# Performance work log

Hardware: AMD Instinct MI355X
Metric: run time of the kernel (lower is better)

The kernel has to match this reference:

```python
import jax, jax.numpy as jnp
import numpy as np

DIM = 1024
NH = 8
HD = DIM // NH  # 128
E = 8
EPS = 1e-5


def rope_cos_sin(L, hd):
    # matches RotaryPositionEmbedding: emb = cat([freqs, freqs], -1)
    inv_freq = 1.0 / (10000.0 ** (jnp.arange(0, hd, 2, dtype=jnp.float32) / hd))
    freqs = jnp.arange(L, dtype=jnp.float32)[:, None] * inv_freq[None, :]  # (L, hd/2)
    emb = jnp.concatenate([freqs, freqs], axis=-1)  # (L, hd)
    return jnp.cos(emb), jnp.sin(emb)


def rotate_half(x):
    # interleaved rotate, as in the torch apply_rope
    x1 = x[..., 0::2]
    x2 = x[..., 1::2]
    return jnp.stack((-x2, x1), axis=-1).reshape(x.shape)


def rope(t, cos, sin):
    # t: (B,H,L,D); cos/sin: (L,D)
    return t * cos[None, None] + rotate_half(t) * sin[None, None]


def heads(t):
    B, L, C = t.shape
    return t.reshape(B, L, NH, HD).transpose(0, 2, 1, 3)  # (B,H,L,D)


def setup_inputs() -> dict:
    key = jax.random.key(0)
    ks = jax.random.split(key, 32)
    std = 0.02
    d = {}
    d['x'] = jax.random.normal(ks[0], (16, 512, DIM), jnp.float32)
    d['h_a'] = jax.random.normal(ks[1], (16, 256, DIM), jnp.float32)
    d['h_t'] = jax.random.normal(ks[2], (16, 256, DIM), jnp.float32)
    names = ['qa', 'ka', 'va', 'qt', 'kt', 'vt', 'o', 'ffn']
    for i, n in enumerate(names):
        d['W_' + n] = jax.random.normal(ks[3 + 2 * i], (E, DIM, DIM), jnp.float32) * std
        d['b_' + n] = jax.random.normal(ks[4 + 2 * i], (E, DIM), jnp.float32) * std
    d['gamma'] = jnp.ones((E, DIM), jnp.float32)
    d['beta'] = jnp.zeros((E, DIM), jnp.float32)
    d['gating_factor'] = jnp.zeros((E,), jnp.float32)
    d['expert_idx'] = 3
    return d


def reference(x, h_a, h_t,
              W_qa, b_qa, W_ka, b_ka, W_va, b_va,
              W_qt, b_qt, W_kt, b_kt, W_vt, b_vt,
              W_o, b_o, W_ffn, b_ffn,
              gamma, beta, gating_factor, expert_idx):
    e = expert_idx

    def lin(t, W, b):
        return t @ W[e].T + b[e]

    B, T, C = x.shape
    Ka = h_a.shape[1]
    Kt = h_t.shape[1]

    q_a = heads(lin(x, W_qa, b_qa))        # (B,H,T,D)
    q_t = heads(lin(x, W_qt, b_qt))
    k_a = heads(lin(h_a, W_ka, b_ka))      # (B,H,Ka,D)
    v_a = heads(lin(h_a, W_va, b_va))
    k_t = heads(lin(h_t, W_kt, b_kt))      # (B,H,Kt,D)
    v_t = heads(lin(h_t, W_vt, b_vt))

    cos_m, sin_m = rope_cos_sin(T, HD)
    q_a = rope(q_a, cos_m, sin_m)
    q_t = rope(q_t, cos_m, sin_m)
    cos_a, sin_a = rope_cos_sin(Ka, HD)
    k_a = rope(k_a, cos_a, sin_a)
    cos_t, sin_t = rope_cos_sin(Kt, HD)
    k_t = rope(k_t, cos_t, sin_t)

    ratio_g = jax.nn.sigmoid(gating_factor[e])
    s_a = jnp.einsum('bhtd,bhkd->bhtk', q_a, k_a)
    s_t = jnp.einsum('bhtd,bhkd->bhtk', q_t, k_t) * ratio_g
    scores = jnp.concatenate([s_a, s_t], axis=-1) / np.sqrt(HD)
    w = jax.nn.softmax(scores, axis=-1)            # (B,H,T,Ka+Kt)
    v = jnp.concatenate([v_a, v_t], axis=2)        # (B,H,Ka+Kt,D)
    out = jnp.einsum('bhtk,bhkd->bhtd', w, v)
    out = out.transpose(0, 2, 1, 3).reshape(B, T, C)
    out = lin(out, W_o, b_o)

    x = out + x
    # ffn: SmileMoENorm -> SmileMoELinear -> ReLU (no extra residual)
    mu = jnp.mean(x, axis=-1, keepdims=True)
    var = jnp.var(x, axis=-1, keepdims=True)
    xn = (x - mu) / jnp.sqrt(var + EPS) * gamma[e] + beta[e]
    x = jax.nn.relu(lin(xn, W_ffn, b_ffn))
    return x
```

## Files before the change

### kernel.cpp

```cpp
#include <hip/hip_runtime.h>
#include <stdint.h>

typedef __bf16 bf16x8 __attribute__((ext_vector_type(8)));
typedef float f32x4 __attribute__((ext_vector_type(4)));
typedef unsigned short u16x8 __attribute__((ext_vector_type(8)));

typedef const __attribute__((address_space(1))) void* gas_ptr;
typedef __attribute__((address_space(3))) void* las_ptr;
typedef const __attribute__((address_space(3))) char* lds_c3;

__device__ __forceinline__ void gload16(const void* g, void* l) {
  __builtin_amdgcn_global_load_lds((gas_ptr)g, (las_ptr)l, 16, 0, 0);
}

__device__ __forceinline__ bf16x8 dsread16(const char* p) {
  bf16x8 r;
  asm volatile("ds_read_b128 %0, %1" : "=v"(r) : "v"((lds_c3)p));
  return r;
}
__device__ __forceinline__ void dswrite2(char* p, uint32_t v) {
  asm volatile("ds_write_b16 %0, %1" : : "v"((las_ptr)p), "v"(v));
}
template <int OFF>
__device__ __forceinline__ float dswz(float x) {
  float r;
  asm volatile("ds_swizzle_b32 %0, %1 offset:%c2" : "=v"(r) : "v"(x), "i"(OFF));
  return r;
}

__device__ __forceinline__ unsigned short f2bf(float f) {
  uint32_t u = __float_as_uint(f);
  u += 0x7FFFu + ((u >> 16) & 1u);
  return (unsigned short)(u >> 16);
}

#define SB __builtin_amdgcn_sched_barrier(0)
#define BAR __builtin_amdgcn_s_barrier()
#define LGK0 asm volatile("s_waitcnt lgkmcnt(0)")

__device__ __forceinline__ void conv8(const float* __restrict__ src,
                                      unsigned short* __restrict__ dst, int i) {
  const float4* s4 = (const float4*)src;
  float4 a = s4[2 * i], b = s4[2 * i + 1];
  u16x8 r;
  r[0] = f2bf(a.x); r[1] = f2bf(a.y); r[2] = f2bf(a.z); r[3] = f2bf(a.w);
  r[4] = f2bf(b.x); r[5] = f2bf(b.y); r[6] = f2bf(b.z); r[7] = f2bf(b.w);
  *(u16x8*)&dst[(size_t)i * 8] = r;
}

__global__ __launch_bounds__(256)
void prep_all(const float* __restrict__ x, const float* __restrict__ h_a,
              const float* __restrict__ h_t,
              const float* W0, const float* W1, const float* W2, const float* W3,
              const float* W4, const float* W5, const float* W6, const float* W7,
              const int* __restrict__ eptr,
              unsigned short* __restrict__ XB, unsigned short* __restrict__ HAB,
              unsigned short* __restrict__ HTB, unsigned short* __restrict__ WW,
              float* __restrict__ cosb, float* __restrict__ sinb) {
  const int blk = blockIdx.x, tid = threadIdx.x;
  if (blk < 4096) {
    conv8(x, XB, blk * 256 + tid);
  } else if (blk < 6144) {
    conv8(h_a, HAB, (blk - 4096) * 256 + tid);
  } else if (blk < 8192) {
    conv8(h_t, HTB, (blk - 6144) * 256 + tid);
  } else if (blk < 12288) {
    const int w = (blk - 8192) >> 9;
    const int i = ((blk - 8192) & 511) * 256 + tid;
    const float* wp;
    switch (w) {
      case 0: wp = W0; break; case 1: wp = W1; break;
      case 2: wp = W2; break; case 3: wp = W3; break;
      case 4: wp = W4; break; case 5: wp = W5; break;
      case 6: wp = W6; break; default: wp = W7; break;
    }
    conv8(wp + (size_t)(*eptr) * 1048576, WW + (size_t)w * 1048576, i);
  } else {
    const int i = (blk - 12288) * 256 + tid;
    const int t = i >> 7, d = i & 127;
    const int f = d & 63;
    float invf = expf(-0.14391156831212787f * (float)f);
    float ang = (float)t * invf;
    float s, c;
    sincosf(ang, &s, &c);
    cosb[i] = c;
    sinb[i] = s;
  }
}

template <int MODE>
__global__ __launch_bounds__(512, 1)
void gemm3r(const unsigned short* __restrict__ A0, const unsigned short* __restrict__ A1,
            const unsigned short* __restrict__ W0, const unsigned short* __restrict__ W1,
            const unsigned short* __restrict__ W2, const unsigned short* __restrict__ W3,
            const float* __restrict__ bias0, const float* __restrict__ bias1,
            const float* __restrict__ bias2, const float* __restrict__ bias3,
            const int* __restrict__ eptr, const float* __restrict__ ctab,
            const float* __restrict__ stab,
            unsigned short* __restrict__ out0, unsigned short* __restrict__ out1,
            unsigned short* __restrict__ outV,
            const float* __restrict__ resid, float* __restrict__ outf) {
  __shared__ __align__(16) char AL[98304];
  __shared__ __align__(16) char BL[49152];
  const int tid = threadIdx.x;
  const int lane = tid & 63, wid = tid >> 6, fr = lane & 15, g = lane >> 4;
  const int wm = wid >> 1, wn = wid & 1;
  const int id = blockIdx.x;
  constexpr int CPX = (MODE == 0) ? 64 : 32;
  const int swz = (id & 7) * CPX + (id >> 3);
  constexpr int NBNS = (MODE <= 1) ? 4 : 3;
  const int bm = swz >> NBNS;
  const int bn = swz & ((1 << NBNS) - 1);
  const int z = (MODE == 1) ? blockIdx.y : 0;
  const int e = *eptr;

  const unsigned short* Asel;
  const unsigned short* Wsel;
  const float* bias;
  int half = 0, cb0;
  if constexpr (MODE == 0) {
    Asel = A0;
    half = bn >> 3;
    Wsel = half ? W1 : W0;
    bias = (half ? bias1 : bias0) + e * 1024;
    cb0 = (bn & 7) * 128;
  } else if constexpr (MODE == 1) {
    Asel = z ? A1 : A0;
    half = bn >> 3;
    Wsel = z ? (half ? W3 : W2) : (half ? W1 : W0);
    bias = (z ? (half ? bias3 : bias2) : (half ? bias1 : bias0)) + e * 1024;
    cb0 = (bn & 7) * 128;
  } else {
    Asel = A0;
    Wsel = W0;
    bias = bias0 + e * 1024;
    cb0 = bn * 128;
  }

  const char* Ab = (const char*)Asel + (size_t)bm * 256 * 2048;
  const char* Bb = (const char*)Wsel + (size_t)cb0 * 2048;

  const int csw = (((tid & 7) ^ ((tid >> 3) & 7)) << 4);
  const char* Ags = Ab + (tid >> 3) * 2048 + csw;
  const char* Bgs = Bb + (tid >> 3) * 2048 + csw;
  char* Ald = AL + tid * 16;
  char* Bld = BL + tid * 16;

#define STA(T, BUF)                                                         \
  { const char* s_ = Ags + (T) * 128;                                       \
    char* d_ = Ald + (BUF) * 32768;                                         \
    gload16(s_, d_);                  gload16(s_ + 131072, d_ + 8192);      \
    gload16(s_ + 262144, d_ + 16384); gload16(s_ + 393216, d_ + 24576); }
#define STB(T, BUF)                                                         \
  { const char* s_ = Bgs + (T) * 128;                                       \
    char* d_ = Bld + (BUF) * 16384;                                         \
    gload16(s_, d_);                  gload16(s_ + 131072, d_ + 8192); }

  const int lsw7 = fr & 7;
  const int ksel = (wid & 4) ? 4 : 0;
  const int cA = ((ksel + g) ^ lsw7) << 4;
  const int cB = (((4 - ksel) + g) ^ lsw7) << 4;
  const int arow = (wm * 64 + fr) * 128;
  const int brow = (wn * 64 + fr) * 128;

  f32x4 acc[4][4];
#pragma unroll
  for (int m = 0; m < 4; ++m)
#pragma unroll
    for (int n = 0; n < 4; ++n) acc[m][n] = f32x4{0.f, 0.f, 0.f, 0.f};
  bf16x8 af[4], bf[4];

#define RDAB(BASEA, BASEB, C)                                               \
  { const char* pa_ = (BASEA) + arow + (C);                                 \
    const char* pb_ = (BASEB) + brow + (C);                                 \
    _Pragma("unroll") for (int m = 0; m < 4; ++m)                           \
        af[m] = dsread16(pa_ + m * 2048);                                   \
    _Pragma("unroll") for (int n = 0; n < 4; ++n)                           \
        bf[n] = dsread16(pb_ + n * 2048); }

#define MF16                                                                \
  __builtin_amdgcn_s_setprio(1);                                            \
  _Pragma("unroll") for (int m = 0; m < 4; ++m)                             \
    _Pragma("unroll") for (int n = 0; n < 4; ++n)                           \
        acc[m][n] = __builtin_amdgcn_mfma_f32_16x16x32_bf16(                \
            af[m], bf[n], acc[m][n], 0, 0, 0);                              \
  __builtin_amdgcn_s_setprio(0);

  STA(0, 0); STB(0, 0); STA(1, 1); STB(1, 1);

  int bc = 0;
#pragma unroll 1
  for (int t = 0; t < 16; ++t) {
    SB;
    if (t <= 14) asm volatile("s_waitcnt vmcnt(6)");
    else         asm volatile("s_waitcnt vmcnt(0)");
    BAR; SB;
    const char* ALc = AL + bc * 32768;
    const char* BLc = BL + bc * 16384;
    const int bs = bc ? bc - 1 : 2;
    RDAB(ALc, BLc, cA); SB;
    if (t <= 13) STA(t + 2, bs);
    SB; LGK0; SB;
    MF16 SB;
    RDAB(ALc, BLc, cB); SB;
    if (t <= 13) STB(t + 2, bs);
    SB; LGK0; SB;
    MF16 SB;
    bc = (bc == 2) ? 0 : bc + 1;
  }
#undef RDAB
#undef MF16
#undef STA
#undef STB

  const int wrow0 = bm * 256 + wm * 64;
#pragma unroll
  for (int m = 0; m < 4; ++m) {
#pragma unroll
    for (int n = 0; n < 4; ++n) {
      const int lc = wn * 64 + n * 16 + fr;
      const int gc = cb0 + lc;
      const float bv = bias[gc];
#pragma unroll
      for (int j = 0; j < 4; ++j) {
        const int grow = wrow0 + m * 16 + g * 4 + j;
        float v = acc[m][n][j] + bv;
        if constexpr (MODE == 0) {
          const int t = grow & 511, bb = grow >> 9;
          const int hh = gc >> 7, dd = gc & 127;
          float pv = __shfl_xor(v, 1);
          float cs = ctab[t * 128 + dd], sn = stab[t * 128 + dd];
          float rh = (dd & 1) ? pv : -pv;
          float o = v * cs + rh * sn;
          unsigned short* dst = half ? out1 : out0;
          dst[(((size_t)(bb * 8 + hh) * 512 + t) << 7) + dd] = f2bf(o);
        } else if constexpr (MODE == 1) {
          const int t = grow & 255, bb = grow >> 8;
          const int hh = gc >> 7, dd = gc & 127;
          if (half == 0) {
            float pv = __shfl_xor(v, 1);
            float cs = ctab[t * 128 + dd], sn = stab[t * 128 + dd];
            float rh = (dd & 1) ? pv : -pv;
            float o = v * cs + rh * sn;
            unsigned short* dst = z ? out1 : out0;
            dst[(((size_t)(bb * 8 + hh) * 256 + t) << 7) + dd] = f2bf(o);
          } else {
            outV[(((size_t)(bb * 8 + hh) << 7) + dd) * 512 + z * 256 + t] = f2bf(v);
          }
        } else {
          const size_t idx = ((size_t)grow << 10) + gc;
          if constexpr (MODE == 2) outf[idx] = v + resid[idx];
          else outf[idx] = fmaxf(v, 0.f);
        }
      }
    }
  }
}

__global__ __launch_bounds__(256, 2)
void attn_kernel(const unsigned short* __restrict__ QA, const unsigned short* __restrict__ QT,
                 const unsigned short* __restrict__ KA, const unsigned short* __restrict__ KT,
                 const unsigned short* __restrict__ VT,
                 unsigned short* __restrict__ AO,
                 const float* __restrict__ gating, const int* __restrict__ eptr) {
  __shared__ unsigned short Ks[2][8192];
  __shared__ unsigned short Vs[2][8192];
  __shared__ unsigned short Ps[8192];
  const int tid = threadIdx.x, lane = tid & 63, wv = tid >> 6;
  const int fr = lane & 15, g = lane >> 4;
  const int bid = blockIdx.x;
  const int b = bid >> 5, h = (bid >> 2) & 7, q0 = (bid & 3) << 7;
  const float ratio = 1.f / (1.f + __expf(-gating[*eptr]));
  const float SC = 0.08838834764831845f;
  const size_t bh = (size_t)(b * 8 + h);

  bf16x8 qf[2][4];
  {
    const char* qa = (const char*)QA + ((bh * 512 + q0 + wv * 32 + fr) << 8) + g * 16;
#pragma unroll
    for (int mb = 0; mb < 2; ++mb)
#pragma unroll
      for (int kb = 0; kb < 4; ++kb)
        qf[mb][kb] = *(const bf16x8*)(qa + mb * 4096 + kb * 64);
  }

  auto stage = [&](int t, int buf) {
    const char* kgb = (const char*)((t < 4) ? KA : KT) + ((bh * 256 + ((size_t)(t & 3) << 6)) << 8);
    const char* vgb = (const char*)VT + (bh << 17) + (t << 7);
    char* ksd = (char*)Ks[buf] + tid * 16;
    char* vsd = (char*)Vs[buf] + tid * 16;
#pragma unroll
    for (int j = 0; j < 4; ++j) {
      const int rk = j * 16 + (tid >> 4);
      const int ck = ((tid & 15) << 4) ^ ((rk & 7) << 4);
      gload16(kgb + rk * 256 + ck, ksd + j * 4096);
      const int dv = j * 32 + (tid >> 3);
      const int cv = ((tid & 7) << 4) ^ ((dv & 7) << 4);
      gload16(vgb + dv * 1024 + cv, vsd + j * 4096);
    }
  };

  float m_run[2][4], l_run[2][4];
  f32x4 oacc[2][8];
#pragma unroll
  for (int mb = 0; mb < 2; ++mb) {
#pragma unroll
    for (int j = 0; j < 4; ++j) { m_run[mb][j] = -1e30f; l_run[mb][j] = 0.f; }
#pragma unroll
    for (int db = 0; db < 8; ++db) oacc[mb][db] = f32x4{0.f, 0.f, 0.f, 0.f};
  }

  stage(0, 0);

  for (int it = 0; it < 8; ++it) {
    const int cur = it & 1;
    if (it < 7) stage(it + 1, cur ^ 1);
    SB;
    if (it < 7) asm volatile("s_waitcnt vmcnt(8)");
    else        asm volatile("s_waitcnt vmcnt(0)");
    SB;
    BAR;
    SB;

    if (it == 4) {
      const char* qt = (const char*)QT + ((bh * 512 + q0 + wv * 32 + fr) << 8) + g * 16;
#pragma unroll
      for (int mb = 0; mb < 2; ++mb)
#pragma unroll
        for (int kb = 0; kb < 4; ++kb)
          qf[mb][kb] = *(const bf16x8*)(qt + mb * 4096 + kb * 64);
    }
    const float sc = (it < 4) ? SC : SC * ratio;
    const char* kc = (const char*)Ks[cur];
    const char* vc = (const char*)Vs[cur];

    f32x4 s[2][4];
#pragma unroll
    for (int mb = 0; mb < 2; ++mb)
#pragma unroll
      for (int nb = 0; nb < 4; ++nb) s[mb][nb] = f32x4{0.f, 0.f, 0.f, 0.f};
    bf16x8 kfa[4], kfb[4];
#pragma unroll
    for (int kb = 0; kb < 4; ++kb) {
      const int byt = (fr * 256 + kb * 64 + g * 16) ^ ((fr & 7) << 4);
      kfa[kb] = dsread16(kc + byt);
    }
#pragma unroll
    for (int nb = 0; nb < 4; ++nb) {
      if (nb < 3) {
#pragma unroll
        for (int kb = 0; kb < 4; ++kb) {
          const int r = (nb + 1) * 16 + fr;
          const int byt = (r * 256 + kb * 64 + g * 16) ^ ((r & 7) << 4);
          if (nb & 1) kfa[kb] = dsread16(kc + byt);
          else        kfb[kb] = dsread16(kc + byt);
        }
        asm volatile("s_waitcnt lgkmcnt(4)");
      } else {
        asm volatile("s_waitcnt lgkmcnt(0)");
      }
      SB;
      __builtin_amdgcn_s_setprio(1);
#pragma unroll
      for (int kb = 0; kb < 4; ++kb) {
        bf16x8 kf = (nb & 1) ? kfb[kb] : kfa[kb];
        s[0][nb] = __builtin_amdgcn_mfma_f32_16x16x32_bf16(qf[0][kb], kf, s[0][nb], 0, 0, 0);
        s[1][nb] = __builtin_amdgcn_mfma_f32_16x16x32_bf16(qf[1][kb], kf, s[1][nb], 0, 0, 0);
      }
      __builtin_amdgcn_s_setprio(0);
    }
    SB;

    float red[8];
#pragma unroll
    for (int mb = 0; mb < 2; ++mb)
#pragma unroll
      for (int j = 0; j < 4; ++j) {
        float mx = -1e30f;
#pragma unroll
        for (int nb = 0; nb < 4; ++nb) {
          s[mb][nb][j] *= sc;
          mx = fmaxf(mx, s[mb][nb][j]);
        }
        red[mb * 4 + j] = mx;
      }
#define MAXR(OFF)                                                        \
    { float tmp[8];                                                      \
      _Pragma("unroll") for (int k = 0; k < 8; ++k) tmp[k] = dswz<OFF>(red[k]); \
      asm volatile("s_waitcnt lgkmcnt(0)");                              \
      SB;                                                                \
      _Pragma("unroll") for (int k = 0; k < 8; ++k) red[k] = fmaxf(red[k], tmp[k]); }
    MAXR(0x041F) MAXR(0x081F) MAXR(0x101F) MAXR(0x201F)
#undef MAXR
#pragma unroll
    for (int mb = 0; mb < 2; ++mb)
#pragma unroll
      for (int j = 0; j < 4; ++j) {
        const float mn = fmaxf(m_run[mb][j], red[mb * 4 + j]);
        const float alpha = __expf(m_run[mb][j] - mn);
        m_run[mb][j] = mn;
        l_run[mb][j] *= alpha;
#pragma unroll
        for (int db = 0; db < 8; ++db) oacc[mb][db][j] *= alpha;
      }
#pragma unroll
    for (int mb = 0; mb < 2; ++mb)
#pragma unroll
      for (int nb = 0; nb < 4; ++nb)
#pragma unroll
        for (int j = 0; j < 4; ++j) {
          float p = __expf(s[mb][nb][j] - m_run[mb][j]);
          l_run[mb][j] += p;
          const int r = wv * 32 + mb * 16 + g * 4 + j;
          const int byt = (r * 128 + (nb * 16 + fr) * 2) ^ ((r & 7) << 4);
          dswrite2((char*)Ps + byt, (uint32_t)f2bf(p));
        }

#pragma unroll
    for (int kb2 = 0; kb2 < 2; ++kb2) {
      bf16x8 pf[2], vf[8];
#pragma unroll
      for (int mb = 0; mb < 2; ++mb) {
        const int r = wv * 32 + mb * 16 + fr;
        const int byt = (r * 128 + kb2 * 64 + g * 16) ^ ((r & 7) << 4);
        pf[mb] = dsread16((const char*)Ps + byt);
      }
#pragma unroll
      for (int db = 0; db < 8; ++db) {
        const int rv = db * 16 + fr;
        const int byt = (rv * 128 + kb2 * 64 + g * 16) ^ ((rv & 7) << 4);
        vf[db] = dsread16(vc + byt);
      }
      asm volatile("s_waitcnt lgkmcnt(0)");
      SB;
      __builtin_amdgcn_s_setprio(1);
#pragma unroll
      for (int db = 0; db < 8; ++db) {
        oacc[0][db] = __builtin_amdgcn_mfma_f32_16x16x32_bf16(pf[0], vf[db], oacc[0][db], 0, 0, 0);
        oacc[1][db] = __builtin_amdgcn_mfma_f32_16x16x32_bf16(pf[1], vf[db], oacc[1][db], 0, 0, 0);
      }
      __builtin_amdgcn_s_setprio(0);
    }
    SB;
    BAR;
  }

#pragma unroll
  for (int mb = 0; mb < 2; ++mb)
#pragma unroll
    for (int j = 0; j < 4; ++j) {
      float lt = l_run[mb][j];
#pragma unroll
      for (int d = 1; d < 16; d <<= 1) lt += __shfl_xor(lt, d);
      float inv = 1.f / lt;
#pragma unroll
      for (int db = 0; db < 8; ++db) {
        float o = oacc[mb][db][j] * inv;
        int row = q0 + wv * 32 + mb * 16 + g * 4 + j;
        int col = h * 128 + db * 16 + fr;
        AO[(((size_t)b * 512 + row) << 10) + col] = f2bf(o);
      }
    }
}

__global__ __launch_bounds__(256)
void ln_kernel(const float* __restrict__ X2, const float* __restrict__ gbase,
               const float* __restrict__ bbase, const int* __restrict__ eptr,
               unsigned short* __restrict__ XN) {
  const int row = blockIdx.x, tid = threadIdx.x;
  const float* x = X2 + ((size_t)row << 10);
  float4 v = ((const float4*)x)[tid];
  float s = v.x + v.y + v.z + v.w;
  float ss = v.x * v.x + v.y * v.y + v.z * v.z + v.w * v.w;
#pragma unroll
  for (int d = 1; d < 64; d <<= 1) {
    s += __shfl_xor(s, d);
    ss += __shfl_xor(ss, d);
  }
  __shared__ float red[8];
  const int wv = tid >> 6, lane = tid & 63;
  if (lane == 0) { red[wv] = s; red[4 + wv] = ss; }
  __syncthreads();
  s = red[0] + red[1] + red[2] + red[3];
  ss = red[4] + red[5] + red[6] + red[7];
  const float mu = s * 0.0009765625f;
  const float var = ss * 0.0009765625f - mu * mu;
  const float inv = rsqrtf(var + 1e-5f);
  const int e = *eptr;
  const float* gg = gbase + e * 1024 + tid * 4;
  const float* bb = bbase + e * 1024 + tid * 4;
  ushort4 o;
  o.x = f2bf((v.x - mu) * inv * gg[0] + bb[0]);
  o.y = f2bf((v.y - mu) * inv * gg[1] + bb[1]);
  o.z = f2bf((v.z - mu) * inv * gg[2] + bb[2]);
  o.w = f2bf((v.w - mu) * inv * gg[3] + bb[3]);
  *(ushort4*)&XN[((size_t)row << 10) + tid * 4] = o;
}

extern "C" void kernel_launch(void* const* d_in, const int* in_sizes, int n_in,
                              void* d_out, int out_size, void* d_ws, size_t ws_size,
                              hipStream_t stream) {
  (void)in_sizes; (void)n_in; (void)out_size; (void)ws_size;
  const float* x      = (const float*)d_in[0];
  const float* h_a    = (const float*)d_in[1];
  const float* h_t    = (const float*)d_in[2];
  const float* W_qa   = (const float*)d_in[3];
  const float* b_qa   = (const float*)d_in[4];
  const float* W_ka   = (const float*)d_in[5];
  const float* b_ka   = (const float*)d_in[6];
  const float* W_va   = (const float*)d_in[7];
  const float* b_va   = (const float*)d_in[8];
  const float* W_qt   = (const float*)d_in[9];
  const float* b_qt   = (const float*)d_in[10];
  const float* W_kt   = (const float*)d_in[11];
  const float* b_kt   = (const float*)d_in[12];
  const float* W_vt   = (const float*)d_in[13];
  const float* b_vt   = (const float*)d_in[14];
  const float* W_o    = (const float*)d_in[15];
  const float* b_o    = (const float*)d_in[16];
  const float* W_ffn  = (const float*)d_in[17];
  const float* b_ffn  = (const float*)d_in[18];
  const float* gamma  = (const float*)d_in[19];
  const float* beta   = (const float*)d_in[20];
  const float* gating = (const float*)d_in[21];
  const int*   eptr   = (const int*)d_in[22];

  char* ws = (char*)d_ws;
  unsigned short* XB  = (unsigned short*)(ws + 0);
  unsigned short* HAB = (unsigned short*)(ws + 16777216);
  unsigned short* HTB = (unsigned short*)(ws + 25165824);
  float*          X2  = (float*)(ws + 0);
  unsigned short* WW  = (unsigned short*)(ws + 33554432);
  unsigned short* QAb = (unsigned short*)(ws + 50331648);
  unsigned short* XN  = QAb;
  unsigned short* QTb = (unsigned short*)(ws + 67108864);
  unsigned short* KAb = (unsigned short*)(ws + 83886080);
  unsigned short* KTb = (unsigned short*)(ws + 92274688);
  unsigned short* VTb = (unsigned short*)(ws + 100663296);
  unsigned short* AOb = (unsigned short*)(ws + 117440512);
  float* COS = (float*)(ws + 134217728);
  float* SIN = (float*)(ws + 134479872);

  prep_all<<<12544, 256, 0, stream>>>(x, h_a, h_t,
      W_qa, W_ka, W_va, W_qt, W_kt, W_vt, W_o, W_ffn, eptr,
      XB, HAB, HTB, WW, COS, SIN);

  gemm3r<0><<<dim3(512), 512, 0, stream>>>(XB, nullptr,
      WW + 0ull * 1048576, WW + 3ull * 1048576, nullptr, nullptr,
      b_qa, b_qt, nullptr, nullptr, eptr, COS, SIN,
      QAb, QTb, nullptr, nullptr, nullptr);

  gemm3r<1><<<dim3(256, 2), 512, 0, stream>>>(HAB, HTB,
      WW + 1ull * 1048576, WW + 2ull * 1048576,
      WW + 4ull * 1048576, WW + 5ull * 1048576,
      b_ka, b_va, b_kt, b_vt, eptr, COS, SIN,
      KAb, KTb, VTb, nullptr, nullptr);

  attn_kernel<<<512, 256, 0, stream>>>(QAb, QTb, KAb, KTb, VTb, AOb, gating, eptr);

  gemm3r<2><<<dim3(256), 512, 0, stream>>>(AOb, nullptr,
      WW + 6ull * 1048576, nullptr, nullptr, nullptr,
      b_o, nullptr, nullptr, nullptr, eptr, nullptr, nullptr,
      nullptr, nullptr, nullptr, x, X2);

  ln_kernel<<<8192, 256, 0, stream>>>(X2, gamma, beta, eptr, XN);

  gemm3r<3><<<dim3(256), 512, 0, stream>>>(XN, nullptr,
      WW + 7ull * 1048576, nullptr, nullptr, nullptr,
      b_ffn, nullptr, nullptr, nullptr, eptr, nullptr, nullptr,
      nullptr, nullptr, nullptr, nullptr, (float*)d_out);
}
```

Baseline: 223.6 us.

## Read K and V fragments directly from global memory in attention kernel

Removes the double-buffered LDS staging of K and V tiles, along with the block barriers and vmcnt waits, in the attention kernel. Each wave now loads its MFMA K and V fragments straight from global memory and relies on L1/L2 caching, since all four waves read the same tiles. This cuts LDS usage and synchronization, which could raise occupancy. The cost is redundant global traffic and exposed load latency, because nothing is prefetched ahead of the MFMAs.

```diff
diff --git a/kernel.cpp b/kernel.cpp
--- a/kernel.cpp
+++ b/kernel.cpp
@@ -263,8 +263,6 @@
                  const unsigned short* __restrict__ VT,
                  unsigned short* __restrict__ AO,
                  const float* __restrict__ gating, const int* __restrict__ eptr) {
-  __shared__ unsigned short Ks[2][8192];
-  __shared__ unsigned short Vs[2][8192];
   __shared__ unsigned short Ps[8192];
   const int tid = threadIdx.x, lane = tid & 63, wv = tid >> 6;
   const int fr = lane & 15, g = lane >> 4;
@@ -284,22 +282,6 @@
         qf[mb][kb] = *(const bf16x8*)(qa + mb * 4096 + kb * 64);
   }
 
-  auto stage = [&](int t, int buf) {
-    const char* kgb = (const char*)((t < 4) ? KA : KT) + ((bh * 256 + ((size_t)(t & 3) << 6)) << 8);
-    const char* vgb = (const char*)VT + (bh << 17) + (t << 7);
-    char* ksd = (char*)Ks[buf] + tid * 16;
-    char* vsd = (char*)Vs[buf] + tid * 16;
-#pragma unroll
-    for (int j = 0; j < 4; ++j) {
-      const int rk = j * 16 + (tid >> 4);
-      const int ck = ((tid & 15) << 4) ^ ((rk & 7) << 4);
-      gload16(kgb + rk * 256 + ck, ksd + j * 4096);
-      const int dv = j * 32 + (tid >> 3);
-      const int cv = ((tid & 7) << 4) ^ ((dv & 7) << 4);
-      gload16(vgb + dv * 1024 + cv, vsd + j * 4096);
-    }
-  };
-
   float m_run[2][4], l_run[2][4];
   f32x4 oacc[2][8];
 #pragma unroll
@@ -310,18 +292,8 @@
     for (int db = 0; db < 8; ++db) oacc[mb][db] = f32x4{0.f, 0.f, 0.f, 0.f};
   }
 
-  stage(0, 0);
-
+#pragma unroll 1
   for (int it = 0; it < 8; ++it) {
-    const int cur = it & 1;
-    if (it < 7) stage(it + 1, cur ^ 1);
-    SB;
-    if (it < 7) asm volatile("s_waitcnt vmcnt(8)");
-    else        asm volatile("s_waitcnt vmcnt(0)");
-    SB;
-    BAR;
-    SB;
-
     if (it == 4) {
       const char* qt = (const char*)QT + ((bh * 512 + q0 + wv * 32 + fr) << 8) + g * 16;
 #pragma unroll
@@ -331,45 +303,27 @@
           qf[mb][kb] = *(const bf16x8*)(qt + mb * 4096 + kb * 64);
     }
     const float sc = (it < 4) ? SC : SC * ratio;
-    const char* kc = (const char*)Ks[cur];
-    const char* vc = (const char*)Vs[cur];
+    const char* Kb = (const char*)((it < 4) ? KA : KT) +
+                     ((size_t)(bh * 256 + ((it & 3) << 6)) << 8);
+    const char* Vb = (const char*)VT + (bh << 17) + (it << 7);
 
     f32x4 s[2][4];
 #pragma unroll
     for (int mb = 0; mb < 2; ++mb)
 #pragma unroll
       for (int nb = 0; nb < 4; ++nb) s[mb][nb] = f32x4{0.f, 0.f, 0.f, 0.f};
-    bf16x8 kfa[4], kfb[4];
-#pragma unroll
-    for (int kb = 0; kb < 4; ++kb) {
-      const int byt = (fr * 256 + kb * 64 + g * 16) ^ ((fr & 7) << 4);
-      kfa[kb] = dsread16(kc + byt);
+#pragma unroll
+    for (int nb = 0; nb < 4; ++nb) {
+      bf16x8 kf[4];
+      const char* kr = Kb + (nb * 16 + fr) * 256 + g * 16;
+#pragma unroll
+      for (int kb = 0; kb < 4; ++kb) kf[kb] = *(const bf16x8*)(kr + kb * 64);
+#pragma unroll
+      for (int kb = 0; kb < 4; ++kb) {
+        s[0][nb] = __builtin_amdgcn_mfma_f32_16x16x32_bf16(qf[0][kb], kf[kb], s[0][nb], 0, 0, 0);
+        s[1][nb] = __builtin_amdgcn_mfma_f32_16x16x32_bf16(qf[1][kb], kf[kb], s[1][nb], 0, 0, 0);
+      }
     }
-#pragma unroll
-    for (int nb = 0; nb < 4; ++nb) {
-      if (nb < 3) {
-#pragma unroll
-        for (int kb = 0; kb < 4; ++kb) {
-          const int r = (nb + 1) * 16 + fr;
-          const int byt = (r * 256 + kb * 64 + g * 16) ^ ((r & 7) << 4);
-          if (nb & 1) kfa[kb] = dsread16(kc + byt);
-          else        kfb[kb] = dsread16(kc + byt);
-        }
-        asm volatile("s_waitcnt lgkmcnt(4)");
-      } else {
-        asm volatile("s_waitcnt lgkmcnt(0)");
-      }
-      SB;
-      __builtin_amdgcn_s_setprio(1);
-#pragma unroll
-      for (int kb = 0; kb < 4; ++kb) {
-        bf16x8 kf = (nb & 1) ? kfb[kb] : kfa[kb];
-        s[0][nb] = __builtin_amdgcn_mfma_f32_16x16x32_bf16(qf[0][kb], kf, s[0][nb], 0, 0, 0);
-        s[1][nb] = __builtin_amdgcn_mfma_f32_16x16x32_bf16(qf[1][kb], kf, s[1][nb], 0, 0, 0);
-      }
-      __builtin_amdgcn_s_setprio(0);
-    }
-    SB;
 
     float red[8];
 #pragma unroll
@@ -420,17 +374,14 @@
     for (int kb2 = 0; kb2 < 2; ++kb2) {
       bf16x8 pf[2], vf[8];
 #pragma unroll
+      for (int db = 0; db < 8; ++db)
+        vf[db] = *(const bf16x8*)(Vb + (db * 16 + fr) * 1024 + kb2 * 64 + g * 16);
+#pragma unroll
       for (int mb = 0; mb < 2; ++mb) {
         const int r = wv * 32 + mb * 16 + fr;
         const int byt = (r * 128 + kb2 * 64 + g * 16) ^ ((r & 7) << 4);
         pf[mb] = dsread16((const char*)Ps + byt);
       }
-#pragma unroll
-      for (int db = 0; db < 8; ++db) {
-        const int rv = db * 16 + fr;
-        const int byt = (rv * 128 + kb2 * 64 + g * 16) ^ ((rv & 7) << 4);
-        vf[db] = dsread16(vc + byt);
-      }
       asm volatile("s_waitcnt lgkmcnt(0)");
       SB;
       __builtin_amdgcn_s_setprio(1);
@@ -442,7 +393,6 @@
       __builtin_amdgcn_s_setprio(0);
     }
     SB;
-    BAR;
   }
 
 #pragma unroll
```

Result: slower. 254.5 us (+13.8%).

## Merge Q and K/V projection GEMMs into one launch and batch LDS reads

Applied to the files above, without the earlier changes.

Combines the Q-projection GEMM (512 blocks) and the K/V-projection GEMM (512 blocks) into a single 1024-block launch that decodes each block's role from a swizzled block id. This removes one kernel launch and its tail, so the two sets of tiles can fill the GPU together. The inner loop also now issues both k-halves of LDS reads and both global prefetches before the MFMAs, waiting on a partial lgkmcnt so the second read group overlaps the first MFMA batch. The cost is twice as many fragment registers in a kernel already launched at one block per CU, plus more branching in the epilogue.

```diff
diff --git a/kernel.cpp b/kernel.cpp
--- a/kernel.cpp
+++ b/kernel.cpp
@@ -91,13 +91,17 @@
 template <int MODE>
 __global__ __launch_bounds__(512, 1)
 void gemm3r(const unsigned short* __restrict__ A0, const unsigned short* __restrict__ A1,
+            const unsigned short* __restrict__ A2,
             const unsigned short* __restrict__ W0, const unsigned short* __restrict__ W1,
             const unsigned short* __restrict__ W2, const unsigned short* __restrict__ W3,
+            const unsigned short* __restrict__ W4, const unsigned short* __restrict__ W5,
             const float* __restrict__ bias0, const float* __restrict__ bias1,
             const float* __restrict__ bias2, const float* __restrict__ bias3,
+            const float* __restrict__ bias4, const float* __restrict__ bias5,
             const int* __restrict__ eptr, const float* __restrict__ ctab,
             const float* __restrict__ stab,
-            unsigned short* __restrict__ out0, unsigned short* __restrict__ out1,
+            unsigned short* __restrict__ oQA, unsigned short* __restrict__ oQT,
+            unsigned short* __restrict__ oKA, unsigned short* __restrict__ oKT,
             unsigned short* __restrict__ outV,
             const float* __restrict__ resid, float* __restrict__ outf) {
   __shared__ __align__(16) char AL[98304];
@@ -106,35 +110,36 @@
   const int lane = tid & 63, wid = tid >> 6, fr = lane & 15, g = lane >> 4;
   const int wm = wid >> 1, wn = wid & 1;
   const int id = blockIdx.x;
-  constexpr int CPX = (MODE == 0) ? 64 : 32;
-  const int swz = (id & 7) * CPX + (id >> 3);
-  constexpr int NBNS = (MODE <= 1) ? 4 : 3;
-  const int bm = swz >> NBNS;
-  const int bn = swz & ((1 << NBNS) - 1);
-  const int z = (MODE == 1) ? blockIdx.y : 0;
   const int e = *eptr;
 
   const unsigned short* Asel;
   const unsigned short* Wsel;
   const float* bias;
-  int half = 0, cb0;
+  int bm, bn, z = 0, half = 0, cb0;
+  bool isQ = true;
   if constexpr (MODE == 0) {
-    Asel = A0;
+    const int swz = (id & 7) * 128 + (id >> 3);
+    if (swz < 512) {
+      bm = swz >> 4; bn = swz & 15;
+    } else {
+      isQ = false;
+      const int s2 = swz - 512;
+      z = s2 >> 8;
+      bm = (s2 & 255) >> 4; bn = s2 & 15;
+    }
     half = bn >> 3;
-    Wsel = half ? W1 : W0;
-    bias = (half ? bias1 : bias0) + e * 1024;
     cb0 = (bn & 7) * 128;
-  } else if constexpr (MODE == 1) {
-    Asel = z ? A1 : A0;
-    half = bn >> 3;
-    Wsel = z ? (half ? W3 : W2) : (half ? W1 : W0);
-    bias = (z ? (half ? bias3 : bias2) : (half ? bias1 : bias0)) + e * 1024;
-    cb0 = (bn & 7) * 128;
+    Asel = isQ ? A0 : (z ? A2 : A1);
+    Wsel = isQ ? (half ? W1 : W0) : (z ? (half ? W5 : W4) : (half ? W3 : W2));
+    bias = (isQ ? (half ? bias1 : bias0)
+                : (z ? (half ? bias5 : bias4) : (half ? bias3 : bias2))) + e * 1024;
   } else {
+    const int swz = (id & 7) * 32 + (id >> 3);
+    bm = swz >> 3; bn = swz & 7;
+    cb0 = bn * 128;
     Asel = A0;
     Wsel = W0;
     bias = bias0 + e * 1024;
-    cb0 = bn * 128;
   }
 
   const char* Ab = (const char*)Asel + (size_t)bm * 256 * 2048;
@@ -168,22 +173,22 @@
   for (int m = 0; m < 4; ++m)
 #pragma unroll
     for (int n = 0; n < 4; ++n) acc[m][n] = f32x4{0.f, 0.f, 0.f, 0.f};
-  bf16x8 af[4], bf[4];
-
-#define RDAB(BASEA, BASEB, C)                                               \
+  bf16x8 af1[4], bf1[4], af2[4], bf2[4];
+
+#define RDAB(BASEA, BASEB, C, AF, BF)                                       \
   { const char* pa_ = (BASEA) + arow + (C);                                 \
     const char* pb_ = (BASEB) + brow + (C);                                 \
     _Pragma("unroll") for (int m = 0; m < 4; ++m)                           \
-        af[m] = dsread16(pa_ + m * 2048);                                   \
+        AF[m] = dsread16(pa_ + m * 2048);                                   \
     _Pragma("unroll") for (int n = 0; n < 4; ++n)                           \
-        bf[n] = dsread16(pb_ + n * 2048); }
-
-#define MF16                                                                \
+        BF[n] = dsread16(pb_ + n * 2048); }
+
+#define MF16(AF, BF)                                                        \
   __builtin_amdgcn_s_setprio(1);                                            \
   _Pragma("unroll") for (int m = 0; m < 4; ++m)                             \
     _Pragma("unroll") for (int n = 0; n < 4; ++n)                           \
         acc[m][n] = __builtin_amdgcn_mfma_f32_16x16x32_bf16(                \
-            af[m], bf[n], acc[m][n], 0, 0, 0);                              \
+            AF[m], BF[n], acc[m][n], 0, 0, 0);                              \
   __builtin_amdgcn_s_setprio(0);
 
   STA(0, 0); STB(0, 0); STA(1, 1); STB(1, 1);
@@ -198,14 +203,16 @@
     const char* ALc = AL + bc * 32768;
     const char* BLc = BL + bc * 16384;
     const int bs = bc ? bc - 1 : 2;
-    RDAB(ALc, BLc, cA); SB;
-    if (t <= 13) STA(t + 2, bs);
-    SB; LGK0; SB;
-    MF16 SB;
-    RDAB(ALc, BLc, cB); SB;
-    if (t <= 13) STB(t + 2, bs);
-    SB; LGK0; SB;
-    MF16 SB;
+    RDAB(ALc, BLc, cA, af1, bf1);
+    RDAB(ALc, BLc, cB, af2, bf2);
+    SB;
+    if (t <= 13) { STA(t + 2, bs); STB(t + 2, bs); }
+    SB;
+    asm volatile("s_waitcnt lgkmcnt(8)");
+    SB;
+    MF16(af1, bf1) SB;
+    LGK0; SB;
+    MF16(af2, bf2) SB;
     bc = (bc == 2) ? 0 : bc + 1;
   }
 #undef RDAB
@@ -226,26 +233,27 @@
         const int grow = wrow0 + m * 16 + g * 4 + j;
         float v = acc[m][n][j] + bv;
         if constexpr (MODE == 0) {
-          const int t = grow & 511, bb = grow >> 9;
           const int hh = gc >> 7, dd = gc & 127;
-          float pv = __shfl_xor(v, 1);
-          float cs = ctab[t * 128 + dd], sn = stab[t * 128 + dd];
-          float rh = (dd & 1) ? pv : -pv;
-          float o = v * cs + rh * sn;
-          unsigned short* dst = half ? out1 : out0;
-          dst[(((size_t)(bb * 8 + hh) * 512 + t) << 7) + dd] = f2bf(o);
-        } else if constexpr (MODE == 1) {
-          const int t = grow & 255, bb = grow >> 8;
-          const int hh = gc >> 7, dd = gc & 127;
-          if (half == 0) {
+          if (isQ) {
+            const int tt = grow & 511, bb = grow >> 9;
             float pv = __shfl_xor(v, 1);
-            float cs = ctab[t * 128 + dd], sn = stab[t * 128 + dd];
+            float cs = ctab[tt * 128 + dd], sn = stab[tt * 128 + dd];
             float rh = (dd & 1) ? pv : -pv;
             float o = v * cs + rh * sn;
-            unsigned short* dst = z ? out1 : out0;
-            dst[(((size_t)(bb * 8 + hh) * 256 + t) << 7) + dd] = f2bf(o);
+            unsigned short* dst = half ? oQT : oQA;
+            dst[(((size_t)(bb * 8 + hh) * 512 + tt) << 7) + dd] = f2bf(o);
           } else {
-            outV[(((size_t)(bb * 8 + hh) << 7) + dd) * 512 + z * 256 + t] = f2bf(v);
+            const int tt = grow & 255, bb = grow >> 8;
+            if (half == 0) {
+              float pv = __shfl_xor(v, 1);
+              float cs = ctab[tt * 128 + dd], sn = stab[tt * 128 + dd];
+              float rh = (dd & 1) ? pv : -pv;
+              float o = v * cs + rh * sn;
+              unsigned short* dst = z ? oKT : oKA;
+              dst[(((size_t)(bb * 8 + hh) * 256 + tt) << 7) + dd] = f2bf(o);
+            } else {
+              outV[(((size_t)(bb * 8 + hh) << 7) + dd) * 512 + z * 256 + tt] = f2bf(v);
+            }
           }
         } else {
           const size_t idx = ((size_t)grow << 10) + gc;
@@ -545,28 +553,27 @@
       W_qa, W_ka, W_va, W_qt, W_kt, W_vt, W_o, W_ffn, eptr,
       XB, HAB, HTB, WW, COS, SIN);
 
-  gemm3r<0><<<dim3(512), 512, 0, stream>>>(XB, nullptr,
-      WW + 0ull * 1048576, WW + 3ull * 1048576, nullptr, nullptr,
-      b_qa, b_qt, nullptr, nullptr, eptr, COS, SIN,
-      QAb, QTb, nullptr, nullptr, nullptr);
-
-  gemm3r<1><<<dim3(256, 2), 512, 0, stream>>>(HAB, HTB,
+  gemm3r<0><<<dim3(1024), 512, 0, stream>>>(XB, HAB, HTB,
+      WW + 0ull * 1048576, WW + 3ull * 1048576,
       WW + 1ull * 1048576, WW + 2ull * 1048576,
       WW + 4ull * 1048576, WW + 5ull * 1048576,
-      b_ka, b_va, b_kt, b_vt, eptr, COS, SIN,
-      KAb, KTb, VTb, nullptr, nullptr);
+      b_qa, b_qt, b_ka, b_va, b_kt, b_vt,
+      eptr, COS, SIN,
+      QAb, QTb, KAb, KTb, VTb, nullptr, nullptr);
 
   attn_kernel<<<512, 256, 0, stream>>>(QAb, QTb, KAb, KTb, VTb, AOb, gating, eptr);
 
-  gemm3r<2><<<dim3(256), 512, 0, stream>>>(AOb, nullptr,
-      WW + 6ull * 1048576, nullptr, nullptr, nullptr,
-      b_o, nullptr, nullptr, nullptr, eptr, nullptr, nullptr,
-      nullptr, nullptr, nullptr, x, X2);
+  gemm3r<2><<<dim3(256), 512, 0, stream>>>(AOb, nullptr, nullptr,
+      WW + 6ull * 1048576, nullptr, nullptr, nullptr, nullptr, nullptr,
+      b_o, nullptr, nullptr, nullptr, nullptr, nullptr,
+      eptr, nullptr, nullptr,
+      nullptr, nullptr, nullptr, nullptr, nullptr, x, X2);
 
   ln_kernel<<<8192, 256, 0, stream>>>(X2, gamma, beta, eptr, XN);
 
-  gemm3r<3><<<dim3(256), 512, 0, stream>>>(XN, nullptr,
-      WW + 7ull * 1048576, nullptr, nullptr, nullptr,
-      b_ffn, nullptr, nullptr, nullptr, eptr, nullptr, nullptr,
-      nullptr, nullptr, nullptr, nullptr, (float*)d_out);
-}
+  gemm3r<3><<<dim3(256), 512, 0, stream>>>(XN, nullptr, nullptr,
+      WW + 7ull * 1048576, nullptr, nullptr, nullptr, nullptr, nullptr,
+      b_ffn, nullptr, nullptr, nullptr, nullptr, nullptr,
+      eptr, nullptr, nullptr,
+      nullptr, nullptr, nullptr, nullptr, nullptr, nullptr, (float*)d_out);
+}
```

After: 259.3 us. +15.9%, slower.

## Use simple 128x128 tile GEMM kernel for QKV projections with RoPE epilogue

Applied to the files above, without the earlier changes.

Replaces the large 256x128 multi-buffered pipelined gemm3r for the Q and K/V projection launches with a new simpler gemm_bt kernel using 128x128 tiles, 256 threads, K-step 32, single-buffered LDS and two barriers per step. This raises the block count and occupancy (launch bounds of 4 blocks per CU) for these GEMMs, at the cost of losing software pipelining and the LDS swizzle, so bank conflicts and load latency may be more exposed. gemm3r is simplified to serve only the output and FFN projections.

```diff
diff --git a/kernel.cpp b/kernel.cpp
--- a/kernel.cpp
+++ b/kernel.cpp
@@ -89,16 +89,115 @@
 }
 
 template <int MODE>
+__global__ __launch_bounds__(256, 4)
+void gemm_bt(const unsigned short* __restrict__ A0, const unsigned short* __restrict__ A1,
+             const unsigned short* __restrict__ W0, const unsigned short* __restrict__ W1,
+             const unsigned short* __restrict__ W2, const unsigned short* __restrict__ W3,
+             const float* __restrict__ b0, const float* __restrict__ b1,
+             const float* __restrict__ b2, const float* __restrict__ b3,
+             const int* __restrict__ eptr, const float* __restrict__ ctab,
+             const float* __restrict__ stab,
+             unsigned short* __restrict__ o0, unsigned short* __restrict__ o1,
+             unsigned short* __restrict__ oV) {
+  __shared__ unsigned short As[128 * 32];
+  __shared__ unsigned short Bs[128 * 32];
+  const int tid = threadIdx.x, lane = tid & 63, wv = tid >> 6;
+  const int wr = wv >> 1, wc = wv & 1;
+  const int bn = blockIdx.x, bm = blockIdx.y;
+  const int z = (MODE == 1) ? blockIdx.z : 0;
+  const int e = *eptr;
+  const int half = bn >> 3;
+  const int cb0 = (bn & 7) * 128;
+
+  const unsigned short* Asel = (MODE == 0) ? A0 : (z ? A1 : A0);
+  const unsigned short* Wsel;
+  const float* bias;
+  if constexpr (MODE == 0) {
+    Wsel = half ? W1 : W0;
+    bias = (half ? b1 : b0) + e * 1024;
+  } else {
+    Wsel = z ? (half ? W3 : W2) : (half ? W1 : W0);
+    bias = (z ? (half ? b3 : b2) : (half ? b1 : b0)) + e * 1024;
+  }
+
+  const int srow = tid >> 2, scol = (tid & 3) << 3;
+  const unsigned short* Ag = Asel + (size_t)(bm * 128 + srow) * 1024 + scol;
+  const unsigned short* Bg = Wsel + (size_t)(cb0 + srow) * 1024 + scol;
+  unsigned short* Asd = As + tid * 8;
+  unsigned short* Bsd = Bs + tid * 8;
+
+  f32x4 acc[4][4];
+#pragma unroll
+  for (int m = 0; m < 4; ++m)
+#pragma unroll
+    for (int n = 0; n < 4; ++n) acc[m][n] = f32x4{0.f, 0.f, 0.f, 0.f};
+
+  const int fr = lane & 15, ko = (lane >> 4) << 3;
+  for (int kt = 0; kt < 1024; kt += 32) {
+    gload16(Ag + kt, Asd);
+    gload16(Ag + kt + 65536, Asd + 2048);
+    gload16(Bg + kt, Bsd);
+    gload16(Bg + kt + 65536, Bsd + 2048);
+    __syncthreads();
+    bf16x8 af[4], bw[4];
+#pragma unroll
+    for (int m = 0; m < 4; ++m)
+      af[m] = *(const bf16x8*)&As[(wr * 64 + m * 16 + fr) * 32 + ko];
+#pragma unroll
+    for (int n = 0; n < 4; ++n)
+      bw[n] = *(const bf16x8*)&Bs[(wc * 64 + n * 16 + fr) * 32 + ko];
+#pragma unroll
+    for (int m = 0; m < 4; ++m)
+#pragma unroll
+      for (int n = 0; n < 4; ++n)
+        acc[m][n] = __builtin_amdgcn_mfma_f32_16x16x32_bf16(af[m], bw[n], acc[m][n], 0, 0, 0);
+    __syncthreads();
+  }
+
+  const int g = lane >> 4;
+#pragma unroll
+  for (int m = 0; m < 4; ++m) {
+#pragma unroll
+    for (int n = 0; n < 4; ++n) {
+      const int gc = cb0 + wc * 64 + n * 16 + fr;
+      const float bv = bias[gc];
+#pragma unroll
+      for (int j = 0; j < 4; ++j) {
+        const int grow = bm * 128 + wr * 64 + m * 16 + g * 4 + j;
+        float v = acc[m][n][j] + bv;
+        const int hh = gc >> 7, dd = gc & 127;
+        if constexpr (MODE == 0) {
+          const int t = grow & 511, bb = grow >> 9;
+          float pv = __shfl_xor(v, 1);
+          float cs = ctab[t * 128 + dd], sn = stab[t * 128 + dd];
+          float rh = (dd & 1) ? pv : -pv;
+          float o = v * cs + rh * sn;
+          unsigned short* dst = half ? o1 : o0;
+          dst[(((size_t)(bb * 8 + hh) * 512 + t) << 7) + dd] = f2bf(o);
+        } else {
+          const int t = grow & 255, bb = grow >> 8;
+          if (half == 0) {
+            float pv = __shfl_xor(v, 1);
+            float cs = ctab[t * 128 + dd], sn = stab[t * 128 + dd];
+            float rh = (dd & 1) ? pv : -pv;
+            float o = v * cs + rh * sn;
+            unsigned short* dst = z ? o1 : o0;
+            dst[(((size_t)(bb * 8 + hh) * 256 + t) << 7) + dd] = f2bf(o);
+          } else {
+            oV[(((size_t)(bb * 8 + hh) << 7) + dd) * 512 + z * 256 + t] = f2bf(v);
+          }
+        }
+      }
+    }
+  }
+}
+
+template <int MODE>
 __global__ __launch_bounds__(512, 1)
-void gemm3r(const unsigned short* __restrict__ A0, const unsigned short* __restrict__ A1,
-            const unsigned short* __restrict__ W0, const unsigned short* __restrict__ W1,
-            const unsigned short* __restrict__ W2, const unsigned short* __restrict__ W3,
-            const float* __restrict__ bias0, const float* __restrict__ bias1,
-            const float* __restrict__ bias2, const float* __restrict__ bias3,
-            const int* __restrict__ eptr, const float* __restrict__ ctab,
-            const float* __restrict__ stab,
-            unsigned short* __restrict__ out0, unsigned short* __restrict__ out1,
-            unsigned short* __restrict__ outV,
+void gemm3r(const unsigned short* __restrict__ A,
+            const unsigned short* __restrict__ W,
+            const float* __restrict__ bias0,
+            const int* __restrict__ eptr,
             const float* __restrict__ resid, float* __restrict__ outf) {
   __shared__ __align__(16) char AL[98304];
   __shared__ __align__(16) char BL[49152];
@@ -106,39 +205,14 @@
   const int lane = tid & 63, wid = tid >> 6, fr = lane & 15, g = lane >> 4;
   const int wm = wid >> 1, wn = wid & 1;
   const int id = blockIdx.x;
-  constexpr int CPX = (MODE == 0) ? 64 : 32;
-  const int swz = (id & 7) * CPX + (id >> 3);
-  constexpr int NBNS = (MODE <= 1) ? 4 : 3;
-  const int bm = swz >> NBNS;
-  const int bn = swz & ((1 << NBNS) - 1);
-  const int z = (MODE == 1) ? blockIdx.y : 0;
+  const int swz = (id & 7) * 32 + (id >> 3);
+  const int bm = swz >> 3, bn = swz & 7;
   const int e = *eptr;
-
-  const unsigned short* Asel;
-  const unsigned short* Wsel;
-  const float* bias;
-  int half = 0, cb0;
-  if constexpr (MODE == 0) {
-    Asel = A0;
-    half = bn >> 3;
-    Wsel = half ? W1 : W0;
-    bias = (half ? bias1 : bias0) + e * 1024;
-    cb0 = (bn & 7) * 128;
-  } else if constexpr (MODE == 1) {
-    Asel = z ? A1 : A0;
-    half = bn >> 3;
-    Wsel = z ? (half ? W3 : W2) : (half ? W1 : W0);
-    bias = (z ? (half ? bias3 : bias2) : (half ? bias1 : bias0)) + e * 1024;
-    cb0 = (bn & 7) * 128;
-  } else {
-    Asel = A0;
-    Wsel = W0;
-    bias = bias0 + e * 1024;
-    cb0 = bn * 128;
-  }
-
-  const char* Ab = (const char*)Asel + (size_t)bm * 256 * 2048;
-  const char* Bb = (const char*)Wsel + (size_t)cb0 * 2048;
+  const float* bias = bias0 + e * 1024;
+  const int cb0 = bn * 128;
+
+  const char* Ab = (const char*)A + (size_t)bm * 256 * 2048;
+  const char* Bb = (const char*)W + (size_t)cb0 * 2048;
 
   const int csw = (((tid & 7) ^ ((tid >> 3) & 7)) << 4);
   const char* Ags = Ab + (tid >> 3) * 2048 + csw;
@@ -218,40 +292,15 @@
   for (int m = 0; m < 4; ++m) {
 #pragma unroll
     for (int n = 0; n < 4; ++n) {
-      const int lc = wn * 64 + n * 16 + fr;
-      const int gc = cb0 + lc;
+      const int gc = cb0 + wn * 64 + n * 16 + fr;
       const float bv = bias[gc];
 #pragma unroll
       for (int j = 0; j < 4; ++j) {
         const int grow = wrow0 + m * 16 + g * 4 + j;
         float v = acc[m][n][j] + bv;
-        if constexpr (MODE == 0) {
-          const int t = grow & 511, bb = grow >> 9;
-          const int hh = gc >> 7, dd = gc & 127;
-          float pv = __shfl_xor(v, 1);
-          float cs = ctab[t * 128 + dd], sn = stab[t * 128 + dd];
-          float rh = (dd & 1) ? pv : -pv;
-          float o = v * cs + rh * sn;
-          unsigned short* dst = half ? out1 : out0;
-          dst[(((size_t)(bb * 8 + hh) * 512 + t) << 7) + dd] = f2bf(o);
-        } else if constexpr (MODE == 1) {
-          const int t = grow & 255, bb = grow >> 8;
-          const int hh = gc >> 7, dd = gc & 127;
-          if (half == 0) {
-            float pv = __shfl_xor(v, 1);
-            float cs = ctab[t * 128 + dd], sn = stab[t * 128 + dd];
-            float rh = (dd & 1) ? pv : -pv;
-            float o = v * cs + rh * sn;
-            unsigned short* dst = z ? out1 : out0;
-            dst[(((size_t)(bb * 8 + hh) * 256 + t) << 7) + dd] = f2bf(o);
-          } else {
-            outV[(((size_t)(bb * 8 + hh) << 7) + dd) * 512 + z * 256 + t] = f2bf(v);
-          }
-        } else {
-          const size_t idx = ((size_t)grow << 10) + gc;
-          if constexpr (MODE == 2) outf[idx] = v + resid[idx];
-          else outf[idx] = fmaxf(v, 0.f);
-        }
+        const size_t idx = ((size_t)grow << 10) + gc;
+        if constexpr (MODE == 2) outf[idx] = v + resid[idx];
+        else outf[idx] = fmaxf(v, 0.f);
       }
     }
   }
@@ -545,28 +594,23 @@
       W_qa, W_ka, W_va, W_qt, W_kt, W_vt, W_o, W_ffn, eptr,
       XB, HAB, HTB, WW, COS, SIN);
 
-  gemm3r<0><<<dim3(512), 512, 0, stream>>>(XB, nullptr,
+  gemm_bt<0><<<dim3(16, 64), 256, 0, stream>>>(XB, nullptr,
       WW + 0ull * 1048576, WW + 3ull * 1048576, nullptr, nullptr,
       b_qa, b_qt, nullptr, nullptr, eptr, COS, SIN,
-      QAb, QTb, nullptr, nullptr, nullptr);
-
-  gemm3r<1><<<dim3(256, 2), 512, 0, stream>>>(HAB, HTB,
+      QAb, QTb, nullptr);
+
+  gemm_bt<1><<<dim3(16, 32, 2), 256, 0, stream>>>(HAB, HTB,
       WW + 1ull * 1048576, WW + 2ull * 1048576,
       WW + 4ull * 1048576, WW + 5ull * 1048576,
       b_ka, b_va, b_kt, b_vt, eptr, COS, SIN,
-      KAb, KTb, VTb, nullptr, nullptr);
+      KAb, KTb, VTb);
 
   attn_kernel<<<512, 256, 0, stream>>>(QAb, QTb, KAb, KTb, VTb, AOb, gating, eptr);
 
-  gemm3r<2><<<dim3(256), 512, 0, stream>>>(AOb, nullptr,
-      WW + 6ull * 1048576, nullptr, nullptr, nullptr,
-      b_o, nullptr, nullptr, nullptr, eptr, nullptr, nullptr,
-      nullptr, nullptr, nullptr, x, X2);
+  gemm3r<2><<<dim3(256), 512, 0, stream>>>(AOb, WW + 6ull * 1048576, b_o, eptr, x, X2);
 
   ln_kernel<<<8192, 256, 0, stream>>>(X2, gamma, beta, eptr, XN);
 
-  gemm3r<3><<<dim3(256), 512, 0, stream>>>(XN, nullptr,
-      WW + 7ull * 1048576, nullptr, nullptr, nullptr,
-      b_ffn, nullptr, nullptr, nullptr, eptr, nullptr, nullptr,
-      nullptr, nullptr, nullptr, nullptr, (float*)d_out);
-}
+  gemm3r<3><<<dim3(256), 512, 0, stream>>>(XN, WW + 7ull * 1048576, b_ffn, eptr,
+                                           nullptr, (float*)d_out);
+}
```

Result: slower. 237.8 us (+6.4%).
